# Kernel tuning notes

Hardware: AMD Instinct MI355X
Metric: run time of the kernel (lower is better)

## Reference

```python
import jax, jax.numpy as jnp
import numpy as np

DIM = 256
NH = 8
KA = 3
DR = 4
CR = DIM // DR            # 64 reduced dim
CPH = CR // NH            # 8 channels per head
SCALE = (DIM // NH) ** -0.5  # head_dim uses full dim, per original code


def _unfold_kernel():
    # fixed identity depthwise kernel: out channel c*KA*KA+i picks window offset i of channel c
    eye = jnp.eye(KA * KA, dtype=jnp.float32).reshape(KA * KA, 1, KA, KA)
    return jnp.tile(eye, (CPH, 1, 1, 1))  # (KA*KA*CPH, 1, KA, KA)


def _dwconv(x, w, b):
    # x: (N, CPH, H, W), w: (KA*KA*CPH, 1, KA, KA), groups=CPH, 'same' zero padding
    y = jax.lax.conv_general_dilated(
        x, w, window_strides=(1, 1), padding=[(KA // 2, KA // 2)] * 2,
        dimension_numbers=("NCHW", "OIHW", "NCHW"), feature_group_count=CPH)
    return y + b[None, :, None, None]


def setup_inputs() -> dict:
    key = jax.random.key(0)
    ks = jax.random.split(key, 8)
    B, L = 16, 4096
    x = jax.random.normal(ks[0], (B, L, DIM), dtype=jnp.float32)
    qkv_w = jax.random.normal(ks[1], (3 * CR, DIM), dtype=jnp.float32) * 0.02
    qkv_b = jnp.zeros((3 * CR,), dtype=jnp.float32)
    dep_conv_b = jax.random.normal(ks[2], (KA * KA * CPH,), dtype=jnp.float32) * 0.02
    dep_conv1_w = jax.random.normal(ks[3], (KA * KA * CPH, 1, KA, KA), dtype=jnp.float32) * 0.02
    dep_conv1_b = jnp.zeros((KA * KA * CPH,), dtype=jnp.float32)
    rpb_table = jax.random.normal(ks[4], (1, NH, 1, KA * KA, 1, 1), dtype=jnp.float32) * 0.02
    proj_w = jax.random.normal(ks[5], (DIM, CR), dtype=jnp.float32) * 0.02
    proj_b = jnp.zeros((DIM,), dtype=jnp.float32)
    return {
        "x": x, "H22": 64, "W22": 64,
        "relative_pos_index": jax.random.randint(ks[6], (9, 9), 0, 9),
        "relative_coords_table": jax.random.normal(ks[7], (9, 2), dtype=jnp.float32),
        "qkv_w": qkv_w, "qkv_b": qkv_b,
        "dep_conv_b": dep_conv_b, "dep_conv1_w": dep_conv1_w, "dep_conv1_b": dep_conv1_b,
        "rpb_table": rpb_table, "proj_w": proj_w, "proj_b": proj_b,
    }


def reference(x, H22, W22, relative_pos_index, relative_coords_table,
              qkv_w, qkv_b, dep_conv_b, dep_conv1_w, dep_conv1_b,
              rpb_table, proj_w, proj_b):
    B1, L1, C1 = x.shape
    H = int(np.sqrt(L1)); W = H
    # faithful to original: reshape (B,L,C)->(B,C,H,W) then move channels last
    xhw = x.reshape(B1, C1, H, W).transpose(0, 2, 3, 1)       # (B,H,W,C)
    qkv = xhw @ qkv_w.T + qkv_b                               # (B,H,W,3*CR)
    f = qkv.transpose(0, 3, 1, 2).reshape(B1 * NH, 3 * CPH, H, W)
    q = (f[:, :CPH] * SCALE).reshape(B1, NH, CPH, 1, H, W)
    kk = f[:, CPH:2 * CPH]                                    # (B*NH, CPH, H, W)
    vv = f[:, 2 * CPH:]
    w0 = _unfold_kernel()
    k = _dwconv(kk, w0, dep_conv_b) + _dwconv(kk, dep_conv1_w, dep_conv1_b)
    v = _dwconv(vv, w0, dep_conv_b) + _dwconv(vv, dep_conv1_w, dep_conv1_b)
    k = k.reshape(B1, NH, CPH, KA * KA, H, W) + rpb_table     # rpb bias on k
    v = v.reshape(B1, NH, CPH, KA * KA, H, W)
    attn = jax.nn.softmax((q * k).sum(2, keepdims=True), axis=3)  # (B,NH,1,ka*ka,H,W)
    out = (attn * v).sum(3).reshape(B1, CR, H, W).transpose(0, 2, 3, 1)  # (B,H,W,CR)
    out = out @ proj_w.T + proj_b                              # (B,H,W,C1)
    return out.transpose(0, 3, 1, 2).reshape(B1, L1, C1)
```

## Files before the change

### kernel.cpp

```cpp
#include <hip/hip_runtime.h>

#define BB 16
#define HW 4096
#define DIMC 256
#define NHEAD 8
#define CPH 8
#define NQKV 192
#define SCALE 0.17677669529663687f

typedef __attribute__((ext_vector_type(8))) short bf16x8;
typedef __attribute__((ext_vector_type(4))) float f32x4;

__device__ inline unsigned short f2b(float f) {
  union { float f; unsigned int u; } x; x.f = f;
  unsigned int r = x.u + 0x7FFFu + ((x.u >> 16) & 1u);
  return (unsigned short)(r >> 16);
}
__device__ inline float b2f(unsigned short u) {
  union { unsigned int u; float f; } x; x.u = ((unsigned int)u) << 16;
  return x.f;
}
__device__ inline void async_copy16(const void* g, void* l) {
  __builtin_amdgcn_global_load_lds((const __attribute__((address_space(1))) void*)g,
                                   (__attribute__((address_space(3))) void*)l, 16, 0, 0);
}

__global__ __launch_bounds__(256) void cast_xT(const float* __restrict__ x,
                                               unsigned short* __restrict__ xT) {
  __shared__ float Xs[64][69];
  const int b = blockIdx.z;
  const int k0 = blockIdx.y * 64;
  const int s0 = blockIdx.x * 64;
  const int tid = threadIdx.x;
  const float* xb = x + (size_t)b * (DIMC * HW);
#pragma unroll
  for (int i = 0; i < 4; ++i) {
    int idx = tid + i * 256;
    int kr = idx >> 4, f = idx & 15;
    float4 v = *(const float4*)&xb[(size_t)(k0 + kr) * HW + s0 + f * 4];
    Xs[kr][f * 4 + 0] = v.x; Xs[kr][f * 4 + 1] = v.y;
    Xs[kr][f * 4 + 2] = v.z; Xs[kr][f * 4 + 3] = v.w;
  }
  __syncthreads();
  unsigned short* ob = xT + (size_t)b * (HW * DIMC);
#pragma unroll
  for (int i = 0; i < 2; ++i) {
    int slot = tid + i * 256;
    int sr = slot >> 3, g8 = slot & 7;
    unsigned short pk[8];
#pragma unroll
    for (int j = 0; j < 8; ++j) pk[j] = f2b(Xs[g8 * 8 + j][sr]);
    *(uint4*)&ob[(size_t)(s0 + sr) * DIMC + k0 + g8 * 8] = *(uint4*)pk;
  }
}

__global__ __launch_bounds__(256) void cast_qw(const float* __restrict__ qw,
                                               unsigned short* __restrict__ qwf) {
  int t = blockIdx.x * 256 + threadIdx.x;
  int lane = t & 63;
  int cell = t >> 6;
  int m = lane & 15, g = lane >> 4;
  int band = cell >> 3, c32 = cell & 7;
  int j = band * 16 + m;
  int k = c32 * 32 + g * 8;
  unsigned short pk[8];
#pragma unroll
  for (int i = 0; i < 8; ++i) pk[i] = f2b(qw[j * 256 + k + i]);
  *(uint4*)&qwf[(size_t)t * 8] = *(uint4*)pk;
}

__global__ __launch_bounds__(256) void cast_pw(const float* __restrict__ pw,
                                               unsigned short* __restrict__ pwf) {
  int t = blockIdx.x * 256 + threadIdx.x;
  int lane = t & 63;
  int cell = t >> 6;
  int m = lane & 15, g = lane >> 4;
  int band = cell >> 1, c32 = cell & 1;
  int d = band * 16 + m;
  int j = c32 * 32 + g * 8;
  unsigned short pk[8];
#pragma unroll
  for (int i = 0; i < 8; ++i) pk[i] = f2b(pw[d * 64 + j + i]);
  *(uint4*)&pwf[(size_t)t * 8] = *(uint4*)pk;
}

__global__ __launch_bounds__(256) void qkv_mfma(const unsigned short* __restrict__ xT,
                                                const unsigned short* __restrict__ qwf,
                                                const float* __restrict__ qb,
                                                unsigned short* __restrict__ qkvt) {
  __shared__ unsigned short Bs[128 * 256];
  const int b = blockIdx.y;
  const int s_blk = blockIdx.x * 128;
  const int tid = threadIdx.x;
  const int wave = tid >> 6, lane = tid & 63;

  {
    const int row_in = lane >> 5, cst = lane & 31;
#pragma unroll
    for (int ii = 0; ii < 16; ++ii) {
      int i = wave * 16 + ii;
      int s_row = 2 * i + row_in;
      int mem_chunk = (cst & 24) | ((cst ^ s_row) & 7);
      const unsigned short* src =
          xT + ((size_t)b * HW + s_blk + s_row) * DIMC + mem_chunk * 8;
      async_copy16(src, (char*)Bs + i * 1024);
    }
  }
  __syncthreads();

  f32x4 acc[3][8];
#pragma unroll
  for (int t = 0; t < 3; ++t)
#pragma unroll
    for (int st = 0; st < 8; ++st) acc[t][st] = (f32x4){0.f, 0.f, 0.f, 0.f};

  const int n = lane & 15, g = lane >> 4;
#pragma unroll
  for (int c32 = 0; c32 < 8; ++c32) {
    bf16x8 af[3];
#pragma unroll
    for (int t = 0; t < 3; ++t) {
      int band = wave * 3 + t;
      af[t] = *(const bf16x8*)(qwf + ((size_t)(band * 8 + c32) * 64 + lane) * 8);
    }
#pragma unroll
    for (int st = 0; st < 8; ++st) {
      int s_row = st * 16 + n;
      int mc = c32 * 4 + g;
      int stc = (mc & 24) | ((mc ^ s_row) & 7);
      bf16x8 bf = *(const bf16x8*)&Bs[s_row * 256 + stc * 8];
#pragma unroll
      for (int t = 0; t < 3; ++t)
        acc[t][st] = __builtin_amdgcn_mfma_f32_16x16x32_bf16(af[t], bf, acc[t][st], 0, 0, 0);
    }
  }

  unsigned short* ob = qkvt + (size_t)b * (NQKV * HW);
#pragma unroll
  for (int t = 0; t < 3; ++t) {
    int j0 = (wave * 3 + t) * 16 + g * 4;
#pragma unroll
    for (int st = 0; st < 8; ++st) {
      int s = s_blk + st * 16 + n;
#pragma unroll
      for (int r = 0; r < 4; ++r) {
        float v = acc[t][st][r] + qb[j0 + r];
        ob[(size_t)(j0 + r) * HW + s] = f2b(v);
      }
    }
  }
}

__global__ __launch_bounds__(512, 2) void attn_kernel(const unsigned short* __restrict__ qkvt,
                                                      const float* __restrict__ dcb,
                                                      const float* __restrict__ w1,
                                                      const float* __restrict__ dc1b,
                                                      const float* __restrict__ rpb,
                                                      unsigned short* __restrict__ aoT) {
  __shared__ float hal[16][10][20];
  __shared__ float plog[8][9][128];
  __shared__ __align__(16) float wA[8][84];
  __shared__ float dsum[72];
  __shared__ float rpbn[9];
  __shared__ unsigned short ot[128][8];

  const int bn = blockIdx.x;
  const int tile = blockIdx.y;
  const int b = bn >> 3, n = bn & 7;
  const int h0 = (tile >> 2) * 8, w0 = (tile & 3) * 16;
  const int tid = threadIdx.x;
  const int c = tid >> 6, lane = tid & 63;
  const int ly = lane >> 4, lx = lane & 15;
  const int s0 = (h0 + ly) * 64 + (w0 + lx);
  const int s1 = s0 + 256;
  const unsigned short* fb = qkvt + ((size_t)b * NQKV + n * 24) * HW;

  for (int e = tid; e < 2880; e += 512) {
    int cb = e / 180;
    int rem = e - cb * 180;
    int y = rem / 18, xx = rem - y * 18;
    int gy = h0 - 1 + y, gx = w0 - 1 + xx;
    float v = 0.f;
    if ((unsigned)gy < 64u && (unsigned)gx < 64u)
      v = b2f(fb[(size_t)(8 + cb) * HW + gy * 64 + gx]);
    hal[cb][y][xx] = v;
  }
  for (int e = tid; e < 648; e += 512) {
    int cc = e / 81;
    wA[cc][e - cc * 81] = w1[e];
  }
  if (tid < 72) dsum[tid] = dcb[tid] + dc1b[tid];
  else if (tid >= 128 && tid < 137) rpbn[tid - 128] = rpb[n * 9 + (tid - 128)];

  float qc0 = SCALE * b2f(fb[(size_t)c * HW + s0]);
  float qc1 = SCALE * b2f(fb[(size_t)c * HW + s1]);
  __syncthreads();

  float Af[81];
#pragma unroll
  for (int i = 0; i < 20; ++i) {
    float4 v = *(const float4*)&wA[c][i * 4];
    Af[i * 4 + 0] = v.x; Af[i * 4 + 1] = v.y;
    Af[i * 4 + 2] = v.z; Af[i * 4 + 3] = v.w;
  }
  Af[80] = wA[c][80];
#pragma unroll
  for (int p = 0; p < 9; ++p) Af[p * 9 + p] += 1.f;

  {
    float2 t[9];
#pragma unroll
    for (int dy = 0; dy < 3; ++dy)
#pragma unroll
      for (int dx = 0; dx < 3; ++dx)
        t[dy * 3 + dx] = make_float2(hal[c][ly + dy][lx + dx],
                                     hal[c][ly + 4 + dy][lx + dx]);
#pragma unroll
    for (int p = 0; p < 9; ++p) {
      float base = dsum[c * 9 + p] + rpbn[p];
      float kx = base, ky = base;
#pragma unroll
      for (int rs = 0; rs < 9; ++rs) {
        kx = fmaf(Af[p * 9 + rs], t[rs].x, kx);
        ky = fmaf(Af[p * 9 + rs], t[rs].y, ky);
      }
      plog[c][p][lane] = qc0 * kx;
      plog[c][p][lane + 64] = qc1 * ky;
    }
  }
  __syncthreads();

  for (int it = tid; it < 1152; it += 512) {
    int p = it >> 7, px = it & 127;
    float sum = plog[0][p][px] + plog[1][p][px] + plog[2][p][px] + plog[3][p][px] +
                plog[4][p][px] + plog[5][p][px] + plog[6][p][px] + plog[7][p][px];
    plog[0][p][px] = sum;
  }
  __syncthreads();

  float ax[9], ay[9];
  {
    float mx = -1e30f, my = -1e30f;
#pragma unroll
    for (int p = 0; p < 9; ++p) {
      ax[p] = plog[0][p][lane];
      ay[p] = plog[0][p][lane + 64];
      mx = fmaxf(mx, ax[p]); my = fmaxf(my, ay[p]);
    }
    float dx = 0.f, dy = 0.f;
#pragma unroll
    for (int p = 0; p < 9; ++p) {
      ax[p] = __expf(ax[p] - mx); dx += ax[p];
      ay[p] = __expf(ay[p] - my); dy += ay[p];
    }
    float ix = 1.f / dx, iy = 1.f / dy;
#pragma unroll
    for (int p = 0; p < 9; ++p) { ax[p] *= ix; ay[p] *= iy; }
  }

  {
    float2 t[9];
#pragma unroll
    for (int dy = 0; dy < 3; ++dy)
#pragma unroll
      for (int dx = 0; dx < 3; ++dx)
        t[dy * 3 + dx] = make_float2(hal[8 + c][ly + dy][lx + dx],
                                     hal[8 + c][ly + 4 + dy][lx + dx]);
    float ocx = 0.f, ocy = 0.f;
#pragma unroll
    for (int p = 0; p < 9; ++p) {
      float base = dsum[c * 9 + p];
      float vx = base, vy = base;
#pragma unroll
      for (int rs = 0; rs < 9; ++rs) {
        vx = fmaf(Af[p * 9 + rs], t[rs].x, vx);
        vy = fmaf(Af[p * 9 + rs], t[rs].y, vy);
      }
      ocx = fmaf(ax[p], vx, ocx);
      ocy = fmaf(ay[p], vy, ocy);
    }
    ot[lane][c] = f2b(ocx);
    ot[lane + 64][c] = f2b(ocy);
  }
  __syncthreads();

  if (c < 2) {
    int p = c * 64 + lane;
    uint4 val = *(const uint4*)&ot[p][0];
    int sp = (h0 + (p >> 4)) * 64 + w0 + (p & 15);
    *(uint4*)&aoT[((size_t)b * HW + sp) * 64 + n * 8] = val;
  }
}

__global__ __launch_bounds__(256) void proj_mfma(const unsigned short* __restrict__ aoT,
                                                 const unsigned short* __restrict__ pwf,
                                                 const float* __restrict__ pb,
                                                 float* __restrict__ out) {
  __shared__ unsigned short Bs[128 * 64];
  const int b = blockIdx.y;
  const int s_blk = blockIdx.x * 128;
  const int tid = threadIdx.x;
  const int wave = tid >> 6, lane = tid & 63;

  {
    const int slot = lane & 7, rsub = lane >> 3;
#pragma unroll
    for (int ii = 0; ii < 4; ++ii) {
      int i = wave * 4 + ii;
      int row = 8 * i + rsub;
      int mem_chunk = slot ^ rsub;
      const unsigned short* src =
          aoT + ((size_t)b * HW + s_blk + row) * 64 + mem_chunk * 8;
      async_copy16(src, (char*)Bs + i * 1024);
    }
  }
  __syncthreads();

  f32x4 acc[4][8];
#pragma unroll
  for (int t = 0; t < 4; ++t)
#pragma unroll
    for (int st = 0; st < 8; ++st) acc[t][st] = (f32x4){0.f, 0.f, 0.f, 0.f};

  const int n = lane & 15, g = lane >> 4;
#pragma unroll
  for (int c32 = 0; c32 < 2; ++c32) {
    bf16x8 af[4];
#pragma unroll
    for (int t = 0; t < 4; ++t) {
      int band = wave * 4 + t;
      af[t] = *(const bf16x8*)(pwf + ((size_t)(band * 2 + c32) * 64 + lane) * 8);
    }
#pragma unroll
    for (int st = 0; st < 8; ++st) {
      int s_row = st * 16 + n;
      int mc = c32 * 4 + g;
      int stc = mc ^ (s_row & 7);
      bf16x8 bf = *(const bf16x8*)&Bs[s_row * 64 + stc * 8];
#pragma unroll
      for (int t = 0; t < 4; ++t)
        acc[t][st] = __builtin_amdgcn_mfma_f32_16x16x32_bf16(af[t], bf, acc[t][st], 0, 0, 0);
    }
  }

  float bias[4][4];
#pragma unroll
  for (int t = 0; t < 4; ++t)
#pragma unroll
    for (int r = 0; r < 4; ++r) bias[t][r] = pb[(wave * 4 + t) * 16 + g * 4 + r];

  float* ob = out + ((size_t)b << 20);
#pragma unroll
  for (int t = 0; t < 4; ++t) {
    int d0 = (wave * 4 + t) * 16 + g * 4;
#pragma unroll
    for (int st = 0; st < 8; ++st) {
      int s = s_blk + st * 16 + n;
#pragma unroll
      for (int r = 0; r < 4; ++r)
        ob[(size_t)(d0 + r) * HW + s] = acc[t][st][r] + bias[t][r];
    }
  }
}

extern "C" void kernel_launch(void* const* d_in, const int* in_sizes, int n_in,
                              void* d_out, int out_size, void* d_ws, size_t ws_size,
                              hipStream_t stream) {
  (void)in_sizes; (void)n_in; (void)out_size; (void)ws_size;
  const float* x    = (const float*)d_in[0];
  const float* qw   = (const float*)d_in[5];
  const float* qb   = (const float*)d_in[6];
  const float* dcb  = (const float*)d_in[7];
  const float* w1   = (const float*)d_in[8];
  const float* dc1b = (const float*)d_in[9];
  const float* rpb  = (const float*)d_in[10];
  const float* pw   = (const float*)d_in[11];
  const float* pb   = (const float*)d_in[12];

  unsigned short* qkvt = (unsigned short*)d_ws;
  unsigned short* qwf  = (unsigned short*)((char*)d_ws + 25165824);
  unsigned short* aoT  = (unsigned short*)((char*)d_ws + 25165824);
  unsigned short* xT   = (unsigned short*)((char*)d_ws + 33554432);
  unsigned short* pwf  = (unsigned short*)((char*)d_ws + 33554432);

  cast_qw<<<24, 256, 0, stream>>>(qw, qwf);
  cast_xT<<<dim3(64, 4, BB), 256, 0, stream>>>(x, xT);
  qkv_mfma<<<dim3(32, BB), 256, 0, stream>>>(xT, qwf, qb, qkvt);
  cast_pw<<<8, 256, 0, stream>>>(pw, pwf);
  attn_kernel<<<dim3(BB * NHEAD, 32), 512, 0, stream>>>(qkvt, dcb, w1, dc1b, rpb, aoT);
  proj_mfma<<<dim3(32, BB), 256, 0, stream>>>(aoT, pwf, pb, (float*)d_out);
}
```

Baseline: 225.6 us.

## Fuse x transpose/cast into QKV GEMM and retile attention kernel

```diff
diff --git a/kernel.cpp b/kernel.cpp
--- a/kernel.cpp
+++ b/kernel.cpp
@@ -23,35 +23,6 @@
 __device__ inline void async_copy16(const void* g, void* l) {
   __builtin_amdgcn_global_load_lds((const __attribute__((address_space(1))) void*)g,
                                    (__attribute__((address_space(3))) void*)l, 16, 0, 0);
-}
-
-__global__ __launch_bounds__(256) void cast_xT(const float* __restrict__ x,
-                                               unsigned short* __restrict__ xT) {
-  __shared__ float Xs[64][69];
-  const int b = blockIdx.z;
-  const int k0 = blockIdx.y * 64;
-  const int s0 = blockIdx.x * 64;
-  const int tid = threadIdx.x;
-  const float* xb = x + (size_t)b * (DIMC * HW);
-#pragma unroll
-  for (int i = 0; i < 4; ++i) {
-    int idx = tid + i * 256;
-    int kr = idx >> 4, f = idx & 15;
-    float4 v = *(const float4*)&xb[(size_t)(k0 + kr) * HW + s0 + f * 4];
-    Xs[kr][f * 4 + 0] = v.x; Xs[kr][f * 4 + 1] = v.y;
-    Xs[kr][f * 4 + 2] = v.z; Xs[kr][f * 4 + 3] = v.w;
-  }
-  __syncthreads();
-  unsigned short* ob = xT + (size_t)b * (HW * DIMC);
-#pragma unroll
-  for (int i = 0; i < 2; ++i) {
-    int slot = tid + i * 256;
-    int sr = slot >> 3, g8 = slot & 7;
-    unsigned short pk[8];
-#pragma unroll
-    for (int j = 0; j < 8; ++j) pk[j] = f2b(Xs[g8 * 8 + j][sr]);
-    *(uint4*)&ob[(size_t)(s0 + sr) * DIMC + k0 + g8 * 8] = *(uint4*)pk;
-  }
 }
 
 __global__ __launch_bounds__(256) void cast_qw(const float* __restrict__ qw,
@@ -84,29 +55,46 @@
   *(uint4*)&pwf[(size_t)t * 8] = *(uint4*)pk;
 }
 
-__global__ __launch_bounds__(256) void qkv_mfma(const unsigned short* __restrict__ xT,
-                                                const unsigned short* __restrict__ qwf,
-                                                const float* __restrict__ qb,
-                                                unsigned short* __restrict__ qkvt) {
-  __shared__ unsigned short Bs[128 * 256];
+__global__ __launch_bounds__(256, 2) void qkv_fused(const float* __restrict__ x,
+                                                    const unsigned short* __restrict__ qwf,
+                                                    const float* __restrict__ qb,
+                                                    unsigned short* __restrict__ qkvt) {
+  __shared__ float Xs[2][64 * 128];
   const int b = blockIdx.y;
   const int s_blk = blockIdx.x * 128;
   const int tid = threadIdx.x;
   const int wave = tid >> 6, lane = tid & 63;
-
-  {
-    const int row_in = lane >> 5, cst = lane & 31;
-#pragma unroll
-    for (int ii = 0; ii < 16; ++ii) {
-      int i = wave * 16 + ii;
-      int s_row = 2 * i + row_in;
-      int mem_chunk = (cst & 24) | ((cst ^ s_row) & 7);
-      const unsigned short* src =
-          xT + ((size_t)b * HW + s_blk + s_row) * DIMC + mem_chunk * 8;
-      async_copy16(src, (char*)Bs + i * 1024);
-    }
-  }
-  __syncthreads();
+  const float* xb = x + (size_t)b * (DIMC * HW);
+
+  const int rhalf = lane >> 5, cch = lane & 31;
+
+#define STAGE(CK, BUF)                                                        \
+  {                                                                           \
+    _Pragma("unroll")                                                         \
+    for (int ii = 0; ii < 8; ++ii) {                                          \
+      int a = wave * 8 + ii;                                                  \
+      int row = 2 * a + rhalf;                                                \
+      int g3 = row >> 3;                                                      \
+      int fsw = (g3 & 3) | ((g3 & 1) << 2);                                   \
+      const float* src = xb + (size_t)((CK) * 64 + row) * HW + s_blk +        \
+                         (size_t)((cch ^ fsw) & 31) * 4 - (cch & ~31) * 0;    \
+      async_copy16(src + ((cch & 24) * 4), (char*)&Xs[BUF][0] + a * 1024);    \
+    }                                                                         \
+  }
+#undef STAGE
+
+  auto stage = [&](int ck, int buf) {
+#pragma unroll
+    for (int ii = 0; ii < 8; ++ii) {
+      int a = wave * 8 + ii;
+      int row = 2 * a + rhalf;
+      int g3 = row >> 3;
+      int fsw = (g3 & 3) | ((g3 & 1) << 2);
+      int src_chunk = (cch & 24) | ((cch ^ fsw) & 7);
+      const float* src = xb + (size_t)(ck * 64 + row) * HW + s_blk + src_chunk * 4;
+      async_copy16(src, (char*)&Xs[buf][0] + a * 1024);
+    }
+  };
 
   f32x4 acc[3][8];
 #pragma unroll
@@ -115,23 +103,43 @@
     for (int st = 0; st < 8; ++st) acc[t][st] = (f32x4){0.f, 0.f, 0.f, 0.f};
 
   const int n = lane & 15, g = lane >> 4;
-#pragma unroll
-  for (int c32 = 0; c32 < 8; ++c32) {
-    bf16x8 af[3];
-#pragma unroll
-    for (int t = 0; t < 3; ++t) {
-      int band = wave * 3 + t;
-      af[t] = *(const bf16x8*)(qwf + ((size_t)(band * 8 + c32) * 64 + lane) * 8);
-    }
-#pragma unroll
-    for (int st = 0; st < 8; ++st) {
-      int s_row = st * 16 + n;
-      int mc = c32 * 4 + g;
-      int stc = (mc & 24) | ((mc ^ s_row) & 7);
-      bf16x8 bf = *(const bf16x8*)&Bs[s_row * 256 + stc * 8];
-#pragma unroll
-      for (int t = 0; t < 3; ++t)
-        acc[t][st] = __builtin_amdgcn_mfma_f32_16x16x32_bf16(af[t], bf, acc[t][st], 0, 0, 0);
+
+  stage(0, 0);
+#pragma unroll
+  for (int ck = 0; ck < 4; ++ck) {
+    __syncthreads();
+    if (ck < 3) stage(ck + 1, (ck + 1) & 1);
+    const float* Xc = &Xs[ck & 1][0];
+#pragma unroll
+    for (int kk = 0; kk < 2; ++kk) {
+      const int c32 = ck * 2 + kk;
+      bf16x8 af[3];
+#pragma unroll
+      for (int t = 0; t < 3; ++t) {
+        int band = wave * 3 + t;
+        af[t] = *(const bf16x8*)(qwf + ((size_t)(band * 8 + c32) * 64 + lane) * 8);
+      }
+#pragma unroll
+      for (int st = 0; st < 8; ++st) {
+        const int s_loc = st * 16 + n;
+        const int sc = s_loc >> 2, s3 = s_loc & 3;
+        float tv[8];
+#pragma unroll
+        for (int i = 0; i < 8; ++i) {
+          int k = kk * 32 + g * 8 + i;
+          int g3 = k >> 3;
+          int fsw = (g3 & 3) | ((g3 & 1) << 2);
+          int lc = (sc & 24) | ((sc ^ fsw) & 7);
+          tv[i] = Xc[k * 128 + lc * 4 + s3];
+        }
+        union { unsigned int u[4]; bf16x8 v; } pk;
+#pragma unroll
+        for (int i = 0; i < 4; ++i)
+          pk.u[i] = (unsigned int)f2b(tv[2 * i]) | ((unsigned int)f2b(tv[2 * i + 1]) << 16);
+#pragma unroll
+        for (int t = 0; t < 3; ++t)
+          acc[t][st] = __builtin_amdgcn_mfma_f32_16x16x32_bf16(af[t], pk.v, acc[t][st], 0, 0, 0);
+      }
     }
   }
 
@@ -151,144 +159,163 @@
   }
 }
 
-__global__ __launch_bounds__(512, 2) void attn_kernel(const unsigned short* __restrict__ qkvt,
+__global__ __launch_bounds__(256, 3) void attn_kernel(const unsigned short* __restrict__ qkvt,
                                                       const float* __restrict__ dcb,
                                                       const float* __restrict__ w1,
                                                       const float* __restrict__ dc1b,
                                                       const float* __restrict__ rpb,
                                                       unsigned short* __restrict__ aoT) {
-  __shared__ float hal[16][10][20];
-  __shared__ float plog[8][9][128];
-  __shared__ __align__(16) float wA[8][84];
-  __shared__ float dsum[72];
-  __shared__ float rpbn[9];
-  __shared__ unsigned short ot[128][8];
+  __shared__ float hal[8][34][36];
+  __shared__ float wAc[8][128];
 
   const int bn = blockIdx.x;
   const int tile = blockIdx.y;
   const int b = bn >> 3, n = bn & 7;
-  const int h0 = (tile >> 2) * 8, w0 = (tile & 3) * 16;
+  const int h0 = (tile >> 1) * 32, w0 = (tile & 1) * 32;
   const int tid = threadIdx.x;
-  const int c = tid >> 6, lane = tid & 63;
-  const int ly = lane >> 4, lx = lane & 15;
-  const int s0 = (h0 + ly) * 64 + (w0 + lx);
-  const int s1 = s0 + 256;
+  const int col = tid & 31, rg = tid >> 5;
+  const int R = rg * 4;
   const unsigned short* fb = qkvt + ((size_t)b * NQKV + n * 24) * HW;
 
-  for (int e = tid; e < 2880; e += 512) {
-    int cb = e / 180;
-    int rem = e - cb * 180;
-    int y = rem / 18, xx = rem - y * 18;
-    int gy = h0 - 1 + y, gx = w0 - 1 + xx;
+  for (int e = tid; e < 648; e += 256) {
+    int c = e / 81, idx = e - c * 81;
+    int p = idx / 9, rs = idx - p * 9;
+    wAc[c][p * 12 + rs] = w1[e] + (p == rs ? 1.f : 0.f);
+  }
+  if (tid < 72) {
+    int c = tid / 9, p = tid - c * 9;
+    float base = dcb[tid] + dc1b[tid];
+    wAc[c][108 + p] = base + rpb[n * 9 + p];
+    wAc[c][117 + p] = base;
+  }
+  for (int e = tid; e < 9248; e += 256) {
+    int cb = e / 1156;
+    int r2 = e - cb * 1156;
+    int hy = r2 / 34, hx = r2 - hy * 34;
+    int gy = h0 - 1 + hy, gx = w0 - 1 + hx;
     float v = 0.f;
     if ((unsigned)gy < 64u && (unsigned)gx < 64u)
       v = b2f(fb[(size_t)(8 + cb) * HW + gy * 64 + gx]);
-    hal[cb][y][xx] = v;
-  }
-  for (int e = tid; e < 648; e += 512) {
-    int cc = e / 81;
-    wA[cc][e - cc * 81] = w1[e];
-  }
-  if (tid < 72) dsum[tid] = dcb[tid] + dc1b[tid];
-  else if (tid >= 128 && tid < 137) rpbn[tid - 128] = rpb[n * 9 + (tid - 128)];
-
-  float qc0 = SCALE * b2f(fb[(size_t)c * HW + s0]);
-  float qc1 = SCALE * b2f(fb[(size_t)c * HW + s1]);
+    hal[cb][hy][hx] = v;
+  }
   __syncthreads();
 
-  float Af[81];
-#pragma unroll
-  for (int i = 0; i < 20; ++i) {
-    float4 v = *(const float4*)&wA[c][i * 4];
-    Af[i * 4 + 0] = v.x; Af[i * 4 + 1] = v.y;
-    Af[i * 4 + 2] = v.z; Af[i * 4 + 3] = v.w;
-  }
-  Af[80] = wA[c][80];
-#pragma unroll
-  for (int p = 0; p < 9; ++p) Af[p * 9 + p] += 1.f;
-
-  {
-    float2 t[9];
-#pragma unroll
-    for (int dy = 0; dy < 3; ++dy)
-#pragma unroll
-      for (int dx = 0; dx < 3; ++dx)
-        t[dy * 3 + dx] = make_float2(hal[c][ly + dy][lx + dx],
-                                     hal[c][ly + 4 + dy][lx + dx]);
+  float logit[9][4];
+#pragma unroll
+  for (int p = 0; p < 9; ++p)
+#pragma unroll
+    for (int i = 0; i < 4; ++i) logit[p][i] = 0.f;
+
+  float qn[4];
+#pragma unroll
+  for (int i = 0; i < 4; ++i)
+    qn[i] = SCALE * b2f(fb[(size_t)0 * HW + (h0 + R + i) * 64 + (w0 + col)]);
+#pragma unroll
+  for (int c = 0; c < 8; ++c) {
+    float qv[4];
+#pragma unroll
+    for (int i = 0; i < 4; ++i) qv[i] = qn[i];
+    if (c < 7) {
+#pragma unroll
+      for (int i = 0; i < 4; ++i)
+        qn[i] = SCALE * b2f(fb[(size_t)(c + 1) * HW + (h0 + R + i) * 64 + (w0 + col)]);
+    }
+    float T[6][3];
+#pragma unroll
+    for (int r6 = 0; r6 < 6; ++r6)
+#pragma unroll
+      for (int dx = 0; dx < 3; ++dx) T[r6][dx] = hal[c][R + r6][col + dx];
 #pragma unroll
     for (int p = 0; p < 9; ++p) {
-      float base = dsum[c * 9 + p] + rpbn[p];
-      float kx = base, ky = base;
-#pragma unroll
-      for (int rs = 0; rs < 9; ++rs) {
-        kx = fmaf(Af[p * 9 + rs], t[rs].x, kx);
-        ky = fmaf(Af[p * 9 + rs], t[rs].y, ky);
-      }
-      plog[c][p][lane] = qc0 * kx;
-      plog[c][p][lane + 64] = qc1 * ky;
+      float4 a0 = *(const float4*)&wAc[c][p * 12];
+      float4 a1 = *(const float4*)&wAc[c][p * 12 + 4];
+      float a8 = wAc[c][p * 12 + 8];
+      float A9[9] = {a0.x, a0.y, a0.z, a0.w, a1.x, a1.y, a1.z, a1.w, a8};
+      float dk = wAc[c][108 + p];
+      float kv[4] = {dk, dk, dk, dk};
+#pragma unroll
+      for (int ry = 0; ry < 3; ++ry)
+#pragma unroll
+        for (int rx = 0; rx < 3; ++rx)
+#pragma unroll
+          for (int i = 0; i < 4; ++i)
+            kv[i] = fmaf(A9[ry * 3 + rx], T[i + ry][rx], kv[i]);
+#pragma unroll
+      for (int i = 0; i < 4; ++i) logit[p][i] = fmaf(qv[i], kv[i], logit[p][i]);
     }
   }
   __syncthreads();
 
-  for (int it = tid; it < 1152; it += 512) {
-    int p = it >> 7, px = it & 127;
-    float sum = plog[0][p][px] + plog[1][p][px] + plog[2][p][px] + plog[3][p][px] +
-                plog[4][p][px] + plog[5][p][px] + plog[6][p][px] + plog[7][p][px];
-    plog[0][p][px] = sum;
+  for (int e = tid; e < 9248; e += 256) {
+    int cb = e / 1156;
+    int r2 = e - cb * 1156;
+    int hy = r2 / 34, hx = r2 - hy * 34;
+    int gy = h0 - 1 + hy, gx = w0 - 1 + hx;
+    float v = 0.f;
+    if ((unsigned)gy < 64u && (unsigned)gx < 64u)
+      v = b2f(fb[(size_t)(16 + cb) * HW + gy * 64 + gx]);
+    hal[cb][hy][hx] = v;
+  }
+
+#pragma unroll
+  for (int i = 0; i < 4; ++i) {
+    float m = logit[0][i];
+#pragma unroll
+    for (int p = 1; p < 9; ++p) m = fmaxf(m, logit[p][i]);
+    float den = 0.f;
+#pragma unroll
+    for (int p = 0; p < 9; ++p) {
+      float e = __expf(logit[p][i] - m);
+      logit[p][i] = e;
+      den += e;
+    }
+    float inv = 1.f / den;
+#pragma unroll
+    for (int p = 0; p < 9; ++p) logit[p][i] *= inv;
   }
   __syncthreads();
 
-  float ax[9], ay[9];
-  {
-    float mx = -1e30f, my = -1e30f;
+  float outc[8][4];
+#pragma unroll
+  for (int c = 0; c < 8; ++c)
+#pragma unroll
+    for (int i = 0; i < 4; ++i) outc[c][i] = 0.f;
+#pragma unroll
+  for (int c = 0; c < 8; ++c) {
+    float T[6][3];
+#pragma unroll
+    for (int r6 = 0; r6 < 6; ++r6)
+#pragma unroll
+      for (int dx = 0; dx < 3; ++dx) T[r6][dx] = hal[c][R + r6][col + dx];
 #pragma unroll
     for (int p = 0; p < 9; ++p) {
-      ax[p] = plog[0][p][lane];
-      ay[p] = plog[0][p][lane + 64];
-      mx = fmaxf(mx, ax[p]); my = fmaxf(my, ay[p]);
-    }
-    float dx = 0.f, dy = 0.f;
-#pragma unroll
-    for (int p = 0; p < 9; ++p) {
-      ax[p] = __expf(ax[p] - mx); dx += ax[p];
-      ay[p] = __expf(ay[p] - my); dy += ay[p];
-    }
-    float ix = 1.f / dx, iy = 1.f / dy;
-#pragma unroll
-    for (int p = 0; p < 9; ++p) { ax[p] *= ix; ay[p] *= iy; }
-  }
-
-  {
-    float2 t[9];
-#pragma unroll
-    for (int dy = 0; dy < 3; ++dy)
-#pragma unroll
-      for (int dx = 0; dx < 3; ++dx)
-        t[dy * 3 + dx] = make_float2(hal[8 + c][ly + dy][lx + dx],
-                                     hal[8 + c][ly + 4 + dy][lx + dx]);
-    float ocx = 0.f, ocy = 0.f;
-#pragma unroll
-    for (int p = 0; p < 9; ++p) {
-      float base = dsum[c * 9 + p];
-      float vx = base, vy = base;
-#pragma unroll
-      for (int rs = 0; rs < 9; ++rs) {
-        vx = fmaf(Af[p * 9 + rs], t[rs].x, vx);
-        vy = fmaf(Af[p * 9 + rs], t[rs].y, vy);
-      }
-      ocx = fmaf(ax[p], vx, ocx);
-      ocy = fmaf(ay[p], vy, ocy);
-    }
-    ot[lane][c] = f2b(ocx);
-    ot[lane + 64][c] = f2b(ocy);
-  }
-  __syncthreads();
-
-  if (c < 2) {
-    int p = c * 64 + lane;
-    uint4 val = *(const uint4*)&ot[p][0];
-    int sp = (h0 + (p >> 4)) * 64 + w0 + (p & 15);
-    *(uint4*)&aoT[((size_t)b * HW + sp) * 64 + n * 8] = val;
+      float4 a0 = *(const float4*)&wAc[c][p * 12];
+      float4 a1 = *(const float4*)&wAc[c][p * 12 + 4];
+      float a8 = wAc[c][p * 12 + 8];
+      float A9[9] = {a0.x, a0.y, a0.z, a0.w, a1.x, a1.y, a1.z, a1.w, a8};
+      float dv = wAc[c][117 + p];
+      float vv[4] = {dv, dv, dv, dv};
+#pragma unroll
+      for (int ry = 0; ry < 3; ++ry)
+#pragma unroll
+        for (int rx = 0; rx < 3; ++rx)
+#pragma unroll
+          for (int i = 0; i < 4; ++i)
+            vv[i] = fmaf(A9[ry * 3 + rx], T[i + ry][rx], vv[i]);
+#pragma unroll
+      for (int i = 0; i < 4; ++i) outc[c][i] = fmaf(logit[p][i], vv[i], outc[c][i]);
+    }
+  }
+
+#pragma unroll
+  for (int i = 0; i < 4; ++i) {
+    int s = (h0 + R + i) * 64 + (w0 + col);
+    uint4 val;
+    val.x = (unsigned int)f2b(outc[0][i]) | ((unsigned int)f2b(outc[1][i]) << 16);
+    val.y = (unsigned int)f2b(outc[2][i]) | ((unsigned int)f2b(outc[3][i]) << 16);
+    val.z = (unsigned int)f2b(outc[4][i]) | ((unsigned int)f2b(outc[5][i]) << 16);
+    val.w = (unsigned int)f2b(outc[6][i]) | ((unsigned int)f2b(outc[7][i]) << 16);
+    *(uint4*)&aoT[((size_t)b * HW + s) * 64 + n * 8] = val;
   }
 }
 
@@ -380,13 +407,11 @@
   unsigned short* qkvt = (unsigned short*)d_ws;
   unsigned short* qwf  = (unsigned short*)((char*)d_ws + 25165824);
   unsigned short* aoT  = (unsigned short*)((char*)d_ws + 25165824);
-  unsigned short* xT   = (unsigned short*)((char*)d_ws + 33554432);
   unsigned short* pwf  = (unsigned short*)((char*)d_ws + 33554432);
 
   cast_qw<<<24, 256, 0, stream>>>(qw, qwf);
-  cast_xT<<<dim3(64, 4, BB), 256, 0, stream>>>(x, xT);
-  qkv_mfma<<<dim3(32, BB), 256, 0, stream>>>(xT, qwf, qb, qkvt);
   cast_pw<<<8, 256, 0, stream>>>(pw, pwf);
-  attn_kernel<<<dim3(BB * NHEAD, 32), 512, 0, stream>>>(qkvt, dcb, w1, dc1b, rpb, aoT);
+  qkv_fused<<<dim3(32, BB), 256, 0, stream>>>(x, qwf, qb, qkvt);
+  attn_kernel<<<dim3(BB * NHEAD, 4), 256, 0, stream>>>(qkvt, dcb, w1, dc1b, rpb, aoT);
   proj_mfma<<<dim3(32, BB), 256, 0, stream>>>(aoT, pwf, pb, (float*)d_out);
 }
```

New measurement: 734.8 us. 3.26x slower.
